# Kernel optimization log

Measured on AMD Instinct MI355X. Metric: run time of the kernel, lower is better.

The kernel has to match this reference:

```python
import jax, jax.numpy as jnp
import numpy as np

B, L, LOCAL_DIM, M = 4096, 256, 2, 64

def setup_inputs() -> dict:
    key = jax.random.key(0)
    k1, k2 = jax.random.split(key)
    samples = jax.random.randint(k1, (B, L), 0, LOCAL_DIM, dtype=jnp.int32)
    # epsilon near 1 so the product over L=256 sites is numerically stable
    epsilon = 1.0 + 0.05 * jax.random.normal(k2, (LOCAL_DIM, M, L), dtype=jnp.float32)
    return {"samples": samples, "epsilon": epsilon}

def reference(samples, epsilon):
    # samples: (B, L) int occupancies in [0, local_dim)
    # epsilon: (local_dim, M, L)
    # qGPS full path with no_syms: out[b] = sum_m prod_l epsilon[samples[b,l], m, l]
    Ls = samples.shape[-1]
    eps_t = jnp.transpose(epsilon, (2, 0, 1))          # (L, local_dim, M)
    gathered = eps_t[jnp.arange(Ls)[None, :], samples]  # (B, L, M) gather by occupancy
    site_prod = jnp.prod(gathered, axis=1)              # (B, M) product over sites
    return jnp.sum(site_prod, axis=-1)                  # (B,) sum over support dim M
```

## Files before the change

### kernel.cpp

```cpp
#include <hip/hip_runtime.h>

#define BQ 4096
#define LQ 256
#define MQ 64
#define ROWQ 128

__global__ void qgps_transpose_eps(const float* __restrict__ eps,
                                   float* __restrict__ eps_t) {
    int tid = blockIdx.x * blockDim.x + threadIdx.x;
    int m = tid & (MQ - 1);
    int s = (tid >> 6) & 1;
    int l = tid >> 7;
    eps_t[tid] = eps[s * (MQ * LQ) + m * LQ + l];
}

__global__ __launch_bounds__(256) void qgps_kernel(const int* __restrict__ samples,
                                                   const float* __restrict__ eps_t,
                                                   float* __restrict__ out) {
    const int wave = threadIdx.x >> 6;
    const int lane = threadIdx.x & 63;
    const int b = blockIdx.x * 4 + wave;

    const int4* srow4 = (const int4*)(samples + b * LQ);

    float p0 = 1.0f, p1 = 1.0f, p2 = 1.0f, p3 = 1.0f;

#pragma unroll 8
    for (int l4 = 0; l4 < LQ / 4; ++l4) {
        const int4 s4 = srow4[l4];
        const int l = l4 * 4;
        p0 *= eps_t[(l + 0) * ROWQ + s4.x * MQ + lane];
        p1 *= eps_t[(l + 1) * ROWQ + s4.y * MQ + lane];
        p2 *= eps_t[(l + 2) * ROWQ + s4.z * MQ + lane];
        p3 *= eps_t[(l + 3) * ROWQ + s4.w * MQ + lane];
    }
    float p = (p0 * p1) * (p2 * p3);

#pragma unroll
    for (int off = 32; off > 0; off >>= 1)
        p += __shfl_xor(p, off, 64);

    if (lane == 0) out[b] = p;
}

extern "C" void kernel_launch(void* const* d_in, const int* in_sizes, int n_in,
                              void* d_out, int out_size, void* d_ws, size_t ws_size,
                              hipStream_t stream) {
    const int* samples = (const int*)d_in[0];
    const float* eps = (const float*)d_in[1];
    float* out = (float*)d_out;
    float* eps_t = (float*)d_ws;

    qgps_transpose_eps<<<(LQ * 2 * MQ) / 256, 256, 0, stream>>>(eps, eps_t);

    qgps_kernel<<<BQ / 4, 256, 0, stream>>>(samples, eps_t, out);
}
```

Measured before the change: 73.96 us.

## Bit-pack samples and map samples to lanes with wave-uniform epsilon loads

A pre-pass packs each row's occupancies into 64-bit ballot masks, so the sample matrix shrinks to one bit per site. The main kernel now gives each lane a sample and each wave two m indices. Epsilon reads become wave-uniform (scalar-cacheable) loads selected by the sample bit, instead of per-lane gathered loads. Partial sums over m are combined with atomicAdd into a pre-zeroed output, which adds a memset, an extra launch and float atomics whose summation order is nondeterministic. Packing keeps only bit 0, which is valid because local_dim is 2.

```diff
diff --git a/kernel.cpp b/kernel.cpp
--- a/kernel.cpp
+++ b/kernel.cpp
@@ -3,44 +3,57 @@
 #define BQ 4096
 #define LQ 256
 #define MQ 64
-#define ROWQ 128
 
-__global__ void qgps_transpose_eps(const float* __restrict__ eps,
-                                   float* __restrict__ eps_t) {
-    int tid = blockIdx.x * blockDim.x + threadIdx.x;
-    int m = tid & (MQ - 1);
-    int s = (tid >> 6) & 1;
-    int l = tid >> 7;
-    eps_t[tid] = eps[s * (MQ * LQ) + m * LQ + l];
-}
-
-__global__ __launch_bounds__(256) void qgps_kernel(const int* __restrict__ samples,
-                                                   const float* __restrict__ eps_t,
-                                                   float* __restrict__ out) {
+__global__ __launch_bounds__(256) void qgps_pack(const int* __restrict__ samples,
+                                                 unsigned long long* __restrict__ packed) {
     const int wave = threadIdx.x >> 6;
     const int lane = threadIdx.x & 63;
     const int b = blockIdx.x * 4 + wave;
+    const int* row = samples + b * LQ;
+#pragma unroll
+    for (int c2 = 0; c2 < 4; ++c2) {
+        int s = row[c2 * 64 + lane];
+        unsigned long long mask = __ballot(s & 1);
+        if (lane == 0) packed[c2 * BQ + b] = mask;
+    }
+}
 
-    const int4* srow4 = (const int4*)(samples + b * LQ);
+__global__ __launch_bounds__(256) void qgps_main(const unsigned long long* __restrict__ packed,
+                                                 const float* __restrict__ eps,
+                                                 float* __restrict__ out) {
+    const int wave = __builtin_amdgcn_readfirstlane(threadIdx.x >> 6);
+    const int lane = threadIdx.x & 63;
+    const int bg = blockIdx.x >> 3;
+    const int mq = blockIdx.x & 7;
+    const int mc = mq * 4 + wave;
+    const int m0 = mc * 2;
+    const int b = bg * 64 + lane;
 
-    float p0 = 1.0f, p1 = 1.0f, p2 = 1.0f, p3 = 1.0f;
+    const float* e0a = eps + m0 * LQ;
+    const float* e1a = eps + MQ * LQ + m0 * LQ;
+    const float* e0b = e0a + LQ;
+    const float* e1b = e1a + LQ;
 
-#pragma unroll 8
-    for (int l4 = 0; l4 < LQ / 4; ++l4) {
-        const int4 s4 = srow4[l4];
-        const int l = l4 * 4;
-        p0 *= eps_t[(l + 0) * ROWQ + s4.x * MQ + lane];
-        p1 *= eps_t[(l + 1) * ROWQ + s4.y * MQ + lane];
-        p2 *= eps_t[(l + 2) * ROWQ + s4.z * MQ + lane];
-        p3 *= eps_t[(l + 3) * ROWQ + s4.w * MQ + lane];
+    float pa = 1.0f, pb = 1.0f;
+    for (int c2 = 0; c2 < 4; ++c2) {
+        unsigned long long w = packed[c2 * BQ + b];
+        unsigned int wlo = (unsigned int)w;
+        unsigned int whi = (unsigned int)(w >> 32);
+        const int l0 = c2 * 64;
+#pragma unroll 16
+        for (int j = 0; j < 32; ++j) {
+            bool s = (wlo >> j) & 1;
+            pa *= s ? e1a[l0 + j] : e0a[l0 + j];
+            pb *= s ? e1b[l0 + j] : e0b[l0 + j];
+        }
+#pragma unroll 16
+        for (int j = 0; j < 32; ++j) {
+            bool s = (whi >> j) & 1;
+            pa *= s ? e1a[l0 + 32 + j] : e0a[l0 + 32 + j];
+            pb *= s ? e1b[l0 + 32 + j] : e0b[l0 + 32 + j];
+        }
     }
-    float p = (p0 * p1) * (p2 * p3);
-
-#pragma unroll
-    for (int off = 32; off > 0; off >>= 1)
-        p += __shfl_xor(p, off, 64);
-
-    if (lane == 0) out[b] = p;
+    atomicAdd(&out[b], pa + pb);
 }
 
 extern "C" void kernel_launch(void* const* d_in, const int* in_sizes, int n_in,
@@ -49,9 +62,10 @@
     const int* samples = (const int*)d_in[0];
     const float* eps = (const float*)d_in[1];
     float* out = (float*)d_out;
-    float* eps_t = (float*)d_ws;
+    unsigned long long* packed = (unsigned long long*)d_ws;
 
-    qgps_transpose_eps<<<(LQ * 2 * MQ) / 256, 256, 0, stream>>>(eps, eps_t);
+    hipMemsetAsync(out, 0, BQ * sizeof(float), stream);
 
-    qgps_kernel<<<BQ / 4, 256, 0, stream>>>(samples, eps_t, out);
+    qgps_pack<<<BQ / 4, 256, 0, stream>>>(samples, packed);
+    qgps_main<<<512, 256, 0, stream>>>(packed, eps, out);
 }
```

Result: slower. 113.4 us (+53.3%).

## Fuse eps transpose into bit-packed ratio-product qGPS kernel with LDS staging

Applied to the files above, without the earlier changes.

Removes the separate transpose kernel and rewrites the product as prod(eps0) times prod(1 + bit*(eps1/eps0 - 1)). Sample occupancies are packed into ballot bitmasks, the ratio table is staged in padded LDS, and the per-site gather becomes a masked FMA. Each block handles 16 samples and half of M, so global eps traffic drops sharply. Partial sums are combined with atomicAdd, which needs a zeroed output buffer, and the kernel assumes binary occupancies.

```diff
diff --git a/kernel.cpp b/kernel.cpp
--- a/kernel.cpp
+++ b/kernel.cpp
@@ -3,44 +3,112 @@
 #define BQ 4096
 #define LQ 256
 #define MQ 64
-#define ROWQ 128
+#define RSTRIDE 264
 
-__global__ void qgps_transpose_eps(const float* __restrict__ eps,
-                                   float* __restrict__ eps_t) {
-    int tid = blockIdx.x * blockDim.x + threadIdx.x;
-    int m = tid & (MQ - 1);
-    int s = (tid >> 6) & 1;
-    int l = tid >> 7;
-    eps_t[tid] = eps[s * (MQ * LQ) + m * LQ + l];
+__device__ __forceinline__ float bit_and_r(unsigned w, int j, float r) {
+    int msk = __builtin_amdgcn_sbfe((int)w, j, 1);
+    return __uint_as_float(__float_as_uint(r) & (unsigned)msk);
 }
 
-__global__ __launch_bounds__(256) void qgps_kernel(const int* __restrict__ samples,
-                                                   const float* __restrict__ eps_t,
-                                                   float* __restrict__ out) {
-    const int wave = threadIdx.x >> 6;
-    const int lane = threadIdx.x & 63;
-    const int b = blockIdx.x * 4 + wave;
+__global__ __launch_bounds__(256) void qgps_fused(const int* __restrict__ samples,
+                                                  const float* __restrict__ eps,
+                                                  float* __restrict__ out) {
+    __shared__ float rm1[32 * RSTRIDE];
+    __shared__ unsigned long long bits[16 * 4];
+    __shared__ float Cs[32];
+    __shared__ float red[4][16];
 
-    const int4* srow4 = (const int4*)(samples + b * LQ);
-
-    float p0 = 1.0f, p1 = 1.0f, p2 = 1.0f, p3 = 1.0f;
-
-#pragma unroll 8
-    for (int l4 = 0; l4 < LQ / 4; ++l4) {
-        const int4 s4 = srow4[l4];
-        const int l = l4 * 4;
-        p0 *= eps_t[(l + 0) * ROWQ + s4.x * MQ + lane];
-        p1 *= eps_t[(l + 1) * ROWQ + s4.y * MQ + lane];
-        p2 *= eps_t[(l + 2) * ROWQ + s4.z * MQ + lane];
-        p3 *= eps_t[(l + 3) * ROWQ + s4.w * MQ + lane];
-    }
-    float p = (p0 * p1) * (p2 * p3);
+    const int tid = threadIdx.x;
+    const int w = tid >> 6;
+    const int lane = tid & 63;
+    const int bg = blockIdx.x >> 1;
+    const int half = blockIdx.x & 1;
+    const int b0 = bg * 16;
 
 #pragma unroll
-    for (int off = 32; off > 0; off >>= 1)
-        p += __shfl_xor(p, off, 64);
+    for (int i = 0; i < 4; ++i) {
+        const int r = w * 4 + i;
+        const int* row = samples + (b0 + r) * LQ;
+#pragma unroll
+        for (int c2 = 0; c2 < 4; ++c2) {
+            unsigned long long msk = __ballot(row[c2 * 64 + lane] & 1);
+            if (lane == 0) bits[r * 4 + c2] = msk;
+        }
+    }
 
-    if (lane == 0) out[b] = p;
+    const float* e0base = eps + half * 32 * LQ;
+    const float* e1base = eps + (MQ + half * 32) * LQ;
+#pragma unroll 4
+    for (int k = 0; k < 32; ++k) {
+        float a = e0base[k * LQ + tid];
+        float c = e1base[k * LQ + tid];
+        rm1[k * RSTRIDE + tid] = c / a - 1.0f;
+    }
+
+#pragma unroll
+    for (int mm = 0; mm < 8; ++mm) {
+        const int k = w * 8 + mm;
+        const float4 e4 = ((const float4*)(e0base + k * LQ))[lane];
+        float q = (e4.x * e4.y) * (e4.z * e4.w);
+#pragma unroll
+        for (int off = 32; off; off >>= 1) q *= __shfl_xor(q, off, 64);
+        if (lane == 0) Cs[k] = q;
+    }
+    __syncthreads();
+
+    const int b_local = lane >> 2;
+    const int mi = lane & 3;
+    const int k0 = mi + 4 * w;
+    const int k1 = k0 + 16;
+
+    unsigned long long W[4];
+#pragma unroll
+    for (int c2 = 0; c2 < 4; ++c2) W[c2] = bits[b_local * 4 + c2];
+
+    const float4* r0 = (const float4*)&rm1[k0 * RSTRIDE];
+    const float4* r1 = (const float4*)&rm1[k1 * RSTRIDE];
+
+    float p0 = 1.0f, p1 = 1.0f;
+    for (int c2 = 0; c2 < 4; ++c2) {
+        const unsigned lo = (unsigned)W[c2];
+        const unsigned hi = (unsigned)(W[c2] >> 32);
+#pragma unroll
+        for (int q = 0; q < 8; ++q) {
+            float4 ra = r0[c2 * 16 + q];
+            float4 rb = r1[c2 * 16 + q];
+            p0 = fmaf(p0, bit_and_r(lo, 4 * q + 0, ra.x), p0);
+            p1 = fmaf(p1, bit_and_r(lo, 4 * q + 0, rb.x), p1);
+            p0 = fmaf(p0, bit_and_r(lo, 4 * q + 1, ra.y), p0);
+            p1 = fmaf(p1, bit_and_r(lo, 4 * q + 1, rb.y), p1);
+            p0 = fmaf(p0, bit_and_r(lo, 4 * q + 2, ra.z), p0);
+            p1 = fmaf(p1, bit_and_r(lo, 4 * q + 2, rb.z), p1);
+            p0 = fmaf(p0, bit_and_r(lo, 4 * q + 3, ra.w), p0);
+            p1 = fmaf(p1, bit_and_r(lo, 4 * q + 3, rb.w), p1);
+        }
+#pragma unroll
+        for (int q = 0; q < 8; ++q) {
+            float4 ra = r0[c2 * 16 + 8 + q];
+            float4 rb = r1[c2 * 16 + 8 + q];
+            p0 = fmaf(p0, bit_and_r(hi, 4 * q + 0, ra.x), p0);
+            p1 = fmaf(p1, bit_and_r(hi, 4 * q + 0, rb.x), p1);
+            p0 = fmaf(p0, bit_and_r(hi, 4 * q + 1, ra.y), p0);
+            p1 = fmaf(p1, bit_and_r(hi, 4 * q + 1, rb.y), p1);
+            p0 = fmaf(p0, bit_and_r(hi, 4 * q + 2, ra.z), p0);
+            p1 = fmaf(p1, bit_and_r(hi, 4 * q + 2, rb.z), p1);
+            p0 = fmaf(p0, bit_and_r(hi, 4 * q + 3, ra.w), p0);
+            p1 = fmaf(p1, bit_and_r(hi, 4 * q + 3, rb.w), p1);
+        }
+    }
+
+    float s = fmaf(Cs[k0], p0, Cs[k1] * p1);
+    s += __shfl_xor(s, 1, 64);
+    s += __shfl_xor(s, 2, 64);
+    if (mi == 0) red[w][b_local] = s;
+    __syncthreads();
+    if (tid < 16) {
+        float t = (red[0][tid] + red[1][tid]) + (red[2][tid] + red[3][tid]);
+        atomicAdd(&out[b0 + tid], t);
+    }
 }
 
 extern "C" void kernel_launch(void* const* d_in, const int* in_sizes, int n_in,
@@ -49,9 +117,7 @@
     const int* samples = (const int*)d_in[0];
     const float* eps = (const float*)d_in[1];
     float* out = (float*)d_out;
-    float* eps_t = (float*)d_ws;
+    (void)d_ws; (void)ws_size;
 
-    qgps_transpose_eps<<<(LQ * 2 * MQ) / 256, 256, 0, stream>>>(eps, eps_t);
-
-    qgps_kernel<<<BQ / 4, 256, 0, stream>>>(samples, eps_t, out);
+    qgps_fused<<<512, 256, 0, stream>>>(samples, eps, out);
 }
```

New measurement: 70.53 us. -4.6%, faster.

## Compute site products as log-domain bf16 MFMA GEMM with fused weight prep

Applied to the files above, without the earlier changes.

Rewrites the product over sites as exp2 of a matrix product between 0/1 occupancy and log2 differences of epsilon, plus a per-m base sum. Each block builds the log weights in LDS in bf16 and runs 16x16x32 MFMAs, removing the separate transpose kernel and the per-site gather loads. The trade-offs are redundant log computation and eps reads in every block, plus reduced precision from bf16 log weights and the fast log/exp intrinsics.

```diff
diff --git a/kernel.cpp b/kernel.cpp
--- a/kernel.cpp
+++ b/kernel.cpp
@@ -1,46 +1,120 @@
 #include <hip/hip_runtime.h>
 
-#define BQ 4096
 #define LQ 256
 #define MQ 64
-#define ROWQ 128
+#define SW 264
 
-__global__ void qgps_transpose_eps(const float* __restrict__ eps,
-                                   float* __restrict__ eps_t) {
-    int tid = blockIdx.x * blockDim.x + threadIdx.x;
-    int m = tid & (MQ - 1);
-    int s = (tid >> 6) & 1;
-    int l = tid >> 7;
-    eps_t[tid] = eps[s * (MQ * LQ) + m * LQ + l];
+typedef __attribute__((ext_vector_type(8))) short bf16x8;
+typedef __attribute__((ext_vector_type(4))) float f32x4;
+
+#if defined(__has_builtin) && __has_builtin(__builtin_amdgcn_logf)
+#define LOG2F(x) __builtin_amdgcn_logf(x)
+#else
+#define LOG2F(x) __log2f(x)
+#endif
+#if defined(__has_builtin) && __has_builtin(__builtin_amdgcn_exp2f)
+#define EXP2F(x) __builtin_amdgcn_exp2f(x)
+#else
+#define EXP2F(x) exp2f(x)
+#endif
+
+__device__ __forceinline__ unsigned short f2bf(float x) {
+    unsigned u = __float_as_uint(x);
+    u += 0x7FFFu + ((u >> 16) & 1u);
+    return (unsigned short)(u >> 16);
 }
 
-__global__ __launch_bounds__(256) void qgps_kernel(const int* __restrict__ samples,
-                                                   const float* __restrict__ eps_t,
-                                                   float* __restrict__ out) {
-    const int wave = threadIdx.x >> 6;
-    const int lane = threadIdx.x & 63;
-    const int b = blockIdx.x * 4 + wave;
+__global__ __launch_bounds__(256) void qgps_mfma(const int* __restrict__ samples,
+                                                 const float* __restrict__ eps,
+                                                 float* __restrict__ out) {
+    __shared__ __attribute__((aligned(16))) unsigned short Wt[MQ * SW];
+    __shared__ __attribute__((aligned(16))) unsigned short St[16 * SW];
+    __shared__ float bred[MQ * 4];
+    __shared__ float red[4][16];
 
-    const int4* srow4 = (const int4*)(samples + b * LQ);
+    const int tid = threadIdx.x;
+    const int w = tid >> 6;
+    const int lane = tid & 63;
+    const int b0 = blockIdx.x * 16;
 
-    float p0 = 1.0f, p1 = 1.0f, p2 = 1.0f, p3 = 1.0f;
+    {
+        const int m = tid >> 2;
+        const int ls = (tid & 3) * 64;
+        const float4* e0v = (const float4*)(eps + m * LQ + ls);
+        const float4* e1v = (const float4*)(eps + MQ * LQ + m * LQ + ls);
+        unsigned short* wrow = &Wt[m * SW + ls];
+        float acc0 = 0.f;
+#pragma unroll
+        for (int i = 0; i < 16; ++i) {
+            float4 a = e0v[i], c = e1v[i];
+            float l0 = LOG2F(a.x), l1 = LOG2F(a.y);
+            float l2 = LOG2F(a.z), l3 = LOG2F(a.w);
+            acc0 += (l0 + l1) + (l2 + l3);
+            ushort2 p0 = make_ushort2(f2bf(LOG2F(c.x) - l0), f2bf(LOG2F(c.y) - l1));
+            ushort2 p1 = make_ushort2(f2bf(LOG2F(c.z) - l2), f2bf(LOG2F(c.w) - l3));
+            *(ushort2*)&wrow[4 * i] = p0;
+            *(ushort2*)&wrow[4 * i + 2] = p1;
+        }
+        bred[m * 4 + (tid & 3)] = acc0;
+    }
 
-#pragma unroll 8
-    for (int l4 = 0; l4 < LQ / 4; ++l4) {
-        const int4 s4 = srow4[l4];
-        const int l = l4 * 4;
-        p0 *= eps_t[(l + 0) * ROWQ + s4.x * MQ + lane];
-        p1 *= eps_t[(l + 1) * ROWQ + s4.y * MQ + lane];
-        p2 *= eps_t[(l + 2) * ROWQ + s4.z * MQ + lane];
-        p3 *= eps_t[(l + 3) * ROWQ + s4.w * MQ + lane];
+    {
+        const int bl = tid >> 4;
+        const int ls = (tid & 15) * 16;
+        const int4* sp = (const int4*)(samples + (b0 + bl) * LQ + ls);
+        int4 v0 = sp[0], v1 = sp[1], v2 = sp[2], v3 = sp[3];
+        bf16x8 o0, o1;
+        o0[0] = v0.x ? 0x3F80 : 0; o0[1] = v0.y ? 0x3F80 : 0;
+        o0[2] = v0.z ? 0x3F80 : 0; o0[3] = v0.w ? 0x3F80 : 0;
+        o0[4] = v1.x ? 0x3F80 : 0; o0[5] = v1.y ? 0x3F80 : 0;
+        o0[6] = v1.z ? 0x3F80 : 0; o0[7] = v1.w ? 0x3F80 : 0;
+        o1[0] = v2.x ? 0x3F80 : 0; o1[1] = v2.y ? 0x3F80 : 0;
+        o1[2] = v2.z ? 0x3F80 : 0; o1[3] = v2.w ? 0x3F80 : 0;
+        o1[4] = v3.x ? 0x3F80 : 0; o1[5] = v3.y ? 0x3F80 : 0;
+        o1[6] = v3.z ? 0x3F80 : 0; o1[7] = v3.w ? 0x3F80 : 0;
+        *(bf16x8*)&St[bl * SW + ls] = o0;
+        *(bf16x8*)&St[bl * SW + ls + 8] = o1;
     }
-    float p = (p0 * p1) * (p2 * p3);
+    __syncthreads();
 
+    const int fr = lane & 15;
+    const int ko = (lane >> 4) * 8;
+    const unsigned short* Ap = &St[fr * SW + ko];
+    const unsigned short* Bp = &Wt[(w * 16 + fr) * SW + ko];
+    f32x4 acc = {0.f, 0.f, 0.f, 0.f};
 #pragma unroll
-    for (int off = 32; off > 0; off >>= 1)
-        p += __shfl_xor(p, off, 64);
+    for (int k = 0; k < 8; ++k) {
+        bf16x8 af = *(const bf16x8*)(Ap + k * 32);
+        bf16x8 bf = *(const bf16x8*)(Bp + k * 32);
+        acc = __builtin_amdgcn_mfma_f32_16x16x32_bf16(af, bf, acc, 0, 0, 0);
+    }
 
-    if (lane == 0) out[b] = p;
+    const int m = w * 16 + fr;
+    f32x4 bb = *(f32x4*)&bred[m * 4];
+    float base = (bb[0] + bb[1]) + (bb[2] + bb[3]);
+    float t0 = EXP2F(base + acc[0]);
+    float t1 = EXP2F(base + acc[1]);
+    float t2 = EXP2F(base + acc[2]);
+    float t3 = EXP2F(base + acc[3]);
+#pragma unroll
+    for (int off = 1; off < 16; off <<= 1) {
+        t0 += __shfl_xor(t0, off, 64);
+        t1 += __shfl_xor(t1, off, 64);
+        t2 += __shfl_xor(t2, off, 64);
+        t3 += __shfl_xor(t3, off, 64);
+    }
+    if (fr == 0) {
+        const int q = lane >> 4;
+        red[w][q * 4 + 0] = t0;
+        red[w][q * 4 + 1] = t1;
+        red[w][q * 4 + 2] = t2;
+        red[w][q * 4 + 3] = t3;
+    }
+    __syncthreads();
+    if (tid < 16) {
+        float o = (red[0][tid] + red[1][tid]) + (red[2][tid] + red[3][tid]);
+        out[b0 + tid] = o;
+    }
 }
 
 extern "C" void kernel_launch(void* const* d_in, const int* in_sizes, int n_in,
@@ -49,9 +123,7 @@
     const int* samples = (const int*)d_in[0];
     const float* eps = (const float*)d_in[1];
     float* out = (float*)d_out;
-    float* eps_t = (float*)d_ws;
+    (void)d_ws; (void)ws_size;
 
-    qgps_transpose_eps<<<(LQ * 2 * MQ) / 256, 256, 0, stream>>>(eps, eps_t);
-
-    qgps_kernel<<<BQ / 4, 256, 0, stream>>>(samples, eps_t, out);
+    qgps_mfma<<<256, 256, 0, stream>>>(samples, eps, out);
 }
```

Measured after the change: 60.87 us. -17.7%, faster.
